# Kernel optimization log

Hardware: AMD Instinct MI355X
Metric: run time of the kernel (lower is better)

## Reference

```python
import jax, jax.numpy as jnp
import numpy as np

EMSIZE = 2048
NCLASS = 128
D1 = 2
D2 = 2
NSENT = 32768


def setup_inputs() -> dict:
    key = jax.random.key(0)
    k1, k2, k3 = jax.random.split(key, 3)
    x = jax.random.normal(k1, (NSENT, 1, EMSIZE), dtype=jnp.float32)
    # Scaled-normal params (original uses nn.init.normal_; scaling keeps tanh unsaturated)
    W1 = jax.random.normal(k2, (D1 + 1, EMSIZE, NCLASS), dtype=jnp.float32) / np.float32(np.sqrt(EMSIZE))
    b1 = jnp.zeros((1, NCLASS), dtype=jnp.float32)
    W2 = jax.random.normal(k3, (D2 + 1, NCLASS, NCLASS), dtype=jnp.float32) / np.float32(np.sqrt(NCLASS))
    b2 = jnp.zeros((1, NCLASS), dtype=jnp.float32)
    return {"structural_representations": x, "W1": W1, "b1": b1, "W2": W2, "b2": b2}


def _shift_down(y, k, n):
    # y[p] -> y[p-k], zeros for p < k (causal shift along sentence axis)
    return jnp.pad(y, ((k, 0), (0, 0)))[:n] if k > 0 else y


def reference(structural_representations, W1, b1, W2, b2):
    x = structural_representations  # [N, 1, E]
    n, _, e = x.shape
    d1 = W1.shape[0] - 1
    d2 = W2.shape[0] - 1
    c = W1.shape[-1]
    xs = x.reshape(n, e)  # [N, E]

    # Stage 1: S[p] = sum_{k=0..d1, k<=p} (x[p-k] @ W1[k] + b1)
    Y = jnp.einsum('ne,kec->knc', xs, W1)  # [d1+1, N, C]: one big GEMM per tap
    S = sum(_shift_down(Y[k], k, n) for k in range(d1 + 1))  # windowed causal sum
    pos = jnp.arange(n)
    cnt1 = (jnp.minimum(pos, d1) + 1).astype(xs.dtype)  # bias added once per valid tap
    H = jnp.tanh(S + cnt1[:, None] * b1[0])  # [N, C]

    # Stage 2 (i >= d2): Z[i] = sum_{j=0..d2} H[i-d2+j] @ W2[j] + (d2+1)*b2
    G = jnp.einsum('nc,kcd->knd', H, W2)  # [d2+1, N, C]
    Z = sum(_shift_down(G[j], d2 - j, n) for j in range(d2 + 1)) + (d2 + 1) * b2[0]

    # Fallback for i < d2: single term tanh(x[i]@W1[0]+b1) @ W2[0] + b2
    H0 = jnp.tanh(xs @ W1[0] + b1[0])
    Z0 = H0 @ W2[0] + b2[0]
    Z = jnp.where((pos >= d2)[:, None], Z, Z0)

    out = jax.nn.log_softmax(Z, axis=-1)
    return out.reshape(n, 1, c)
```

## Files before the change

### kernel.cpp

```cpp
#include <hip/hip_runtime.h>
#include <math.h>

typedef __attribute__((ext_vector_type(8))) short short8;
typedef __attribute__((ext_vector_type(4))) float f32x4;

#define MFMA16(a, b, c) __builtin_amdgcn_mfma_f32_16x16x32_bf16((a), (b), (c), 0, 0, 0)

__device__ inline void gl_lds16(const void* g, void* l) {
  __builtin_amdgcn_global_load_lds(
      (const __attribute__((address_space(1))) void*)g,
      (__attribute__((address_space(3))) void*)l, 16, 0, 0);
}

__device__ inline unsigned int pack2(float lo, float hi) {
  unsigned int ulo = __float_as_uint(lo), uhi = __float_as_uint(hi);
  return (uhi & 0xFFFF0000u) | (ulo >> 16);
}
__device__ inline unsigned short f2bf_r(float f) {
  return (unsigned short)((__float_as_uint(f) + 0x8000u) >> 16);
}
__device__ inline float bf2f(unsigned short h) {
  return __uint_as_float(((unsigned int)h) << 16);
}

__global__ __launch_bounds__(256) void k_repack_w1(const float* __restrict__ W1,
                                                   unsigned short* __restrict__ W1bt) {
  __shared__ float tile[64 * 128];
  const int b = blockIdx.x;
  const int k = b >> 5, et = b & 31;
  const int e0 = et * 64;
  const int tid = threadIdx.x;
  const float* src = W1 + (size_t)k * 262144 + (size_t)e0 * 128;
#pragma unroll
  for (int i = 0; i < 8; ++i) {
    int idx4 = tid + i * 256;
    ((f32x4*)tile)[idx4] = ((const f32x4*)src)[idx4];
  }
  __syncthreads();
#pragma unroll
  for (int i = 0; i < 4; ++i) {
    int item = tid + i * 256;
    int c = item >> 3, eo = (item & 7) * 8;
    union { unsigned short h[8]; uint4 v; } t;
#pragma unroll
    for (int u = 0; u < 8; ++u) t.h[u] = f2bf_r(tile[(eo + u) * 128 + c]);
    *(uint4*)(W1bt + (size_t)(k * 128 + c) * 2048 + e0 + eo) = t.v;
  }
}

__global__ __launch_bounds__(256) void k_repack_w2(const float* __restrict__ W2,
                                                   unsigned short* __restrict__ W2t) {
  int idx = blockIdx.x * 256 + threadIdx.x;
  int j = idx >> 14, r = idx & 16383, d = r >> 7, c = r & 127;
  W2t[idx] = f2bf_r(W2[(size_t)j * 16384 + (size_t)c * 128 + d]);
}

__global__ __launch_bounds__(256, 2) void k_gemm1(const float* __restrict__ X,
                                                  const unsigned short* __restrict__ Bt,
                                                  unsigned short* __restrict__ Ybf) {
  __shared__ float Alds[64 * 64];
  __shared__ unsigned short Blds[384 * 64];

  const int r0 = blockIdx.x * 64;
  const int tid = threadIdx.x, wave = tid >> 6, lane = tid & 63;
  const int mrow = lane & 15, quad = lane >> 4;

  const float* agp[4];
#pragma unroll
  for (int r = 0; r < 4; ++r) {
    int row = wave * 16 + r * 4 + (lane >> 4);
    int c = (lane & 15) ^ (row & 15);
    agp[r] = X + (size_t)(r0 + row) * 2048 + c * 4;
  }
  const unsigned short* bgp[12];
#pragma unroll
  for (int r = 0; r < 12; ++r) {
    int col = wave * 96 + r * 8 + (lane >> 3);
    int c = (lane & 7) ^ (col & 7);
    bgp[r] = Bt + (size_t)col * 2048 + c * 8;
  }

  f32x4 acc[4][6] = {};

  for (int k0 = 0; k0 < 2048; k0 += 64) {
#pragma unroll
    for (int r = 0; r < 4; ++r)
      gl_lds16(agp[r], (char*)Alds + (wave * 16 + r * 4) * 256);
#pragma unroll
    for (int r = 0; r < 12; ++r)
      gl_lds16(bgp[r], (char*)Blds + (wave * 96 + r * 8) * 128);
#pragma unroll
    for (int r = 0; r < 4; ++r) agp[r] += 64;
#pragma unroll
    for (int r = 0; r < 12; ++r) bgp[r] += 64;
    __syncthreads();

#pragma unroll
    for (int s = 0; s < 2; ++s) {
      short8 af[4];
#pragma unroll
      for (int rt = 0; rt < 4; ++rt) {
        int row = rt * 16 + mrow;
        int c0 = s * 8 + quad * 2;
        const float* base = Alds + row * 64;
        f32x4 x0 = *(const f32x4*)(base + ((c0 ^ mrow) * 4));
        f32x4 x1 = *(const f32x4*)(base + (((c0 + 1) ^ mrow) * 4));
        union { unsigned int u[4]; short8 v; } t;
        t.u[0] = pack2(x0[0], x0[1]); t.u[1] = pack2(x0[2], x0[3]);
        t.u[2] = pack2(x1[0], x1[1]); t.u[3] = pack2(x1[2], x1[3]);
        af[rt] = t.v;
      }
#pragma unroll
      for (int ct = 0; ct < 6; ++ct) {
        int col = wave * 96 + ct * 16 + mrow;
        int ch = (s * 4 + quad) ^ (mrow & 7);
        short8 bf = *(const short8*)(Blds + col * 64 + ch * 8);
#pragma unroll
        for (int rt = 0; rt < 4; ++rt)
          acc[rt][ct] = MFMA16(af[rt], bf, acc[rt][ct]);
      }
    }
    __syncthreads();
  }

#pragma unroll
  for (int rt = 0; rt < 4; ++rt)
#pragma unroll
    for (int ct = 0; ct < 6; ++ct)
#pragma unroll
      for (int rg = 0; rg < 4; ++rg) {
        int rrow = r0 + rt * 16 + quad * 4 + rg;
        int ccol = wave * 96 + ct * 16 + mrow;
        Ybf[(size_t)rrow * 384 + ccol] = f2bf_r(acc[rt][ct][rg]);
      }
}

#define HS 136
__global__ __launch_bounds__(256) void k_stage2(const unsigned short* __restrict__ Yb,
                                                const unsigned short* __restrict__ W2t,
                                                const float* __restrict__ b1,
                                                const float* __restrict__ b2,
                                                float* __restrict__ out) {
  __shared__ unsigned short Hlds[66 * HS];
  __shared__ float zbuf[2][128];
  const int bid = blockIdx.x, tid = threadIdx.x;
  const int r0 = bid * 64;

  for (int idx = tid; idx < 66 * 128; idx += 256) {
    int hl = idx >> 7, c = idx & 127;
    int p = r0 - 2 + hl;
    float h = 0.f;
    if (p >= 0) {
      float s = bf2f(Yb[(size_t)p * 384 + c]);
      float cnt = 1.f;
      if (p >= 1) { s += bf2f(Yb[(size_t)(p - 1) * 384 + 128 + c]); cnt += 1.f; }
      if (p >= 2) { s += bf2f(Yb[(size_t)(p - 2) * 384 + 256 + c]); cnt += 1.f; }
      h = tanhf(fmaf(cnt, b1[c], s));
    }
    Hlds[hl * HS + c] = f2bf_r(h);
  }
  __syncthreads();

  const int wave = tid >> 6, lane = tid & 63, mrow = lane & 15, quad = lane >> 4;
  f32x4 acc[8] = {};
#pragma unroll
  for (int j = 0; j < 3; ++j) {
#pragma unroll
    for (int kk = 0; kk < 4; ++kk) {
      short8 a0 = *(const short8*)&Hlds[(wave * 16 + mrow + j) * HS + kk * 32 + quad * 8];
      const unsigned short* wp = W2t + (size_t)(j * 128 + mrow) * 128 + kk * 32 + quad * 8;
#pragma unroll
      for (int ct = 0; ct < 8; ++ct)
        acc[ct] = MFMA16(a0, *(const short8*)(wp + ct * 16 * 128), acc[ct]);
    }
  }

#pragma unroll
  for (int rg = 0; rg < 4; ++rg) {
    float z[8]; float m = -1e30f;
#pragma unroll
    for (int ct = 0; ct < 8; ++ct) {
      z[ct] = acc[ct][rg] + 3.f * b2[ct * 16 + mrow];
      m = fmaxf(m, z[ct]);
    }
#pragma unroll
    for (int off = 1; off < 16; off <<= 1) m = fmaxf(m, __shfl_xor(m, off, 64));
    float s = 0.f;
#pragma unroll
    for (int ct = 0; ct < 8; ++ct) s += __expf(z[ct] - m);
#pragma unroll
    for (int off = 1; off < 16; off <<= 1) s += __shfl_xor(s, off, 64);
    float lse = m + __logf(s);
    int grow = r0 + wave * 16 + quad * 4 + rg;
    if (grow >= 2) {
      float* op = out + (size_t)grow * 128 + mrow;
#pragma unroll
      for (int ct = 0; ct < 8; ++ct) op[ct * 16] = z[ct] - lse;
    }
  }

  if (bid == 0) {
    __syncthreads();
    int row = tid >> 7, d = tid & 127;
    zbuf[row][d] = tanhf(bf2f(Yb[(size_t)row * 384 + d]) + b1[d]);
    __syncthreads();
    float zv = b2[d];
    for (int c = 0; c < 128; ++c)
      zv = fmaf(zbuf[row][c], bf2f(W2t[(size_t)d * 128 + c]), zv);
    __syncthreads();
    zbuf[row][d] = zv;
    __syncthreads();
    float m = -1e30f;
    for (int c = 0; c < 128; ++c) m = fmaxf(m, zbuf[row][c]);
    float s = 0.f;
    for (int c = 0; c < 128; ++c) s += __expf(zbuf[row][c] - m);
    out[(size_t)row * 128 + d] = zv - m - __logf(s);
  }
}

extern "C" void kernel_launch(void* const* d_in, const int* in_sizes, int n_in,
                              void* d_out, int out_size, void* d_ws, size_t ws_size,
                              hipStream_t stream) {
  const float* X  = (const float*)d_in[0];
  const float* W1 = (const float*)d_in[1];
  const float* b1 = (const float*)d_in[2];
  const float* W2 = (const float*)d_in[3];
  const float* b2 = (const float*)d_in[4];
  float* out = (float*)d_out;

  unsigned short* Ybf  = (unsigned short*)d_ws;
  unsigned short* W1bt = (unsigned short*)((char*)d_ws + 25165824);
  unsigned short* W2t  = (unsigned short*)((char*)d_ws + 25165824 + 1572864);

  k_repack_w1<<<96, 256, 0, stream>>>(W1, W1bt);
  k_repack_w2<<<192, 256, 0, stream>>>(W2, W2t);
  k_gemm1<<<512, 256, 0, stream>>>(X, W1bt, Ybf);
  k_stage2<<<512, 256, 0, stream>>>(Ybf, W2t, b1, b2, out);
}
```

Before: 460.5 us.

## Fuse stage-1 GEMM with stage-2 via recomputed halo rows and merge repack kernels

Merges the GEMM1 and stage-2 kernels into one: each block recomputes 4 extra halo rows of the first GEMM so the causal window and the second GEMM can read Y from LDS. This removes the bf16 Y round trip through global memory (about 25 MB written and read back) and one kernel launch. The two weight repack kernels are also merged into one launch. The cost is 25% more GEMM1 MFMA work per block, more LDS (66 KB), and higher register pressure from the 5x6 accumulators, which can lower occupancy.

```diff
diff --git a/kernel.cpp b/kernel.cpp
--- a/kernel.cpp
+++ b/kernel.cpp
@@ -23,54 +23,66 @@
   return __uint_as_float(((unsigned int)h) << 16);
 }
 
-__global__ __launch_bounds__(256) void k_repack_w1(const float* __restrict__ W1,
-                                                   unsigned short* __restrict__ W1bt) {
+__global__ __launch_bounds__(256) void k_repack(const float* __restrict__ W1,
+                                                const float* __restrict__ W2,
+                                                unsigned short* __restrict__ W1bt,
+                                                unsigned short* __restrict__ W2t) {
   __shared__ float tile[64 * 128];
-  const int b = blockIdx.x;
-  const int k = b >> 5, et = b & 31;
-  const int e0 = et * 64;
-  const int tid = threadIdx.x;
-  const float* src = W1 + (size_t)k * 262144 + (size_t)e0 * 128;
-#pragma unroll
-  for (int i = 0; i < 8; ++i) {
-    int idx4 = tid + i * 256;
-    ((f32x4*)tile)[idx4] = ((const f32x4*)src)[idx4];
-  }
-  __syncthreads();
-#pragma unroll
-  for (int i = 0; i < 4; ++i) {
-    int item = tid + i * 256;
-    int c = item >> 3, eo = (item & 7) * 8;
-    union { unsigned short h[8]; uint4 v; } t;
-#pragma unroll
-    for (int u = 0; u < 8; ++u) t.h[u] = f2bf_r(tile[(eo + u) * 128 + c]);
-    *(uint4*)(W1bt + (size_t)(k * 128 + c) * 2048 + e0 + eo) = t.v;
-  }
-}
-
-__global__ __launch_bounds__(256) void k_repack_w2(const float* __restrict__ W2,
-                                                   unsigned short* __restrict__ W2t) {
-  int idx = blockIdx.x * 256 + threadIdx.x;
-  int j = idx >> 14, r = idx & 16383, d = r >> 7, c = r & 127;
-  W2t[idx] = f2bf_r(W2[(size_t)j * 16384 + (size_t)c * 128 + d]);
-}
-
-__global__ __launch_bounds__(256, 2) void k_gemm1(const float* __restrict__ X,
+  const int b = blockIdx.x, tid = threadIdx.x;
+  if (b < 96) {
+    const int k = b >> 5, et = b & 31;
+    const int e0 = et * 64;
+    const float* src = W1 + (size_t)k * 262144 + (size_t)e0 * 128;
+#pragma unroll
+    for (int i = 0; i < 8; ++i) {
+      int idx4 = tid + i * 256;
+      ((f32x4*)tile)[idx4] = ((const f32x4*)src)[idx4];
+    }
+    __syncthreads();
+#pragma unroll
+    for (int i = 0; i < 4; ++i) {
+      int item = tid + i * 256;
+      int c = item >> 3, eo = (item & 7) * 8;
+      union { unsigned short h[8]; uint4 v; } t;
+#pragma unroll
+      for (int u = 0; u < 8; ++u) t.h[u] = f2bf_r(tile[(eo + u) * 128 + c]);
+      *(uint4*)(W1bt + (size_t)(k * 128 + c) * 2048 + e0 + eo) = t.v;
+    }
+  } else {
+    int idx = (b - 96) * 256 + tid;
+    int j = idx >> 14, r = idx & 16383, d = r >> 7, c = r & 127;
+    W2t[idx] = f2bf_r(W2[(size_t)j * 16384 + (size_t)c * 128 + d]);
+  }
+}
+
+__global__ __launch_bounds__(256, 2) void k_fused(const float* __restrict__ X,
                                                   const unsigned short* __restrict__ Bt,
-                                                  unsigned short* __restrict__ Ybf) {
-  __shared__ float Alds[64 * 64];
-  __shared__ unsigned short Blds[384 * 64];
+                                                  const unsigned short* __restrict__ W2t,
+                                                  const float* __restrict__ b1,
+                                                  const float* __restrict__ b2,
+                                                  float* __restrict__ out) {
+  __shared__ __align__(16) char smem[66560];
+  float* Alds = (float*)smem;
+  unsigned short* Blds = (unsigned short*)(smem + 17408);
+  unsigned short* Yt = (unsigned short*)smem;
+  float* zbuf = (float*)(smem + 62720);
 
   const int r0 = blockIdx.x * 64;
   const int tid = threadIdx.x, wave = tid >> 6, lane = tid & 63;
   const int mrow = lane & 15, quad = lane >> 4;
 
-  const float* agp[4];
+  const float* agp[5];
 #pragma unroll
   for (int r = 0; r < 4; ++r) {
-    int row = wave * 16 + r * 4 + (lane >> 4);
-    int c = (lane & 15) ^ (row & 15);
-    agp[r] = X + (size_t)(r0 + row) * 2048 + c * 4;
+    int i = wave * 16 + r * 4 + (lane >> 4);
+    int g = r0 - 4 + i; if (g < 0) g = 0;
+    int c = (lane & 15) ^ (i & 15);
+    agp[r] = X + (size_t)g * 2048 + c * 4;
+  }
+  {
+    int i = 64 + (lane >> 4);
+    int c = (lane & 15) ^ (i & 15);
+    agp[4] = X + (size_t)(r0 - 4 + i) * 2048 + c * 4;
   }
   const unsigned short* bgp[12];
 #pragma unroll
@@ -80,26 +92,27 @@
     bgp[r] = Bt + (size_t)col * 2048 + c * 8;
   }
 
-  f32x4 acc[4][6] = {};
+  f32x4 acc[5][6] = {};
 
   for (int k0 = 0; k0 < 2048; k0 += 64) {
 #pragma unroll
     for (int r = 0; r < 4; ++r)
       gl_lds16(agp[r], (char*)Alds + (wave * 16 + r * 4) * 256);
+    if (wave == 0) gl_lds16(agp[4], (char*)Alds + 64 * 256);
 #pragma unroll
     for (int r = 0; r < 12; ++r)
       gl_lds16(bgp[r], (char*)Blds + (wave * 96 + r * 8) * 128);
 #pragma unroll
-    for (int r = 0; r < 4; ++r) agp[r] += 64;
+    for (int r = 0; r < 5; ++r) agp[r] += 64;
 #pragma unroll
     for (int r = 0; r < 12; ++r) bgp[r] += 64;
     __syncthreads();
 
 #pragma unroll
     for (int s = 0; s < 2; ++s) {
-      short8 af[4];
-#pragma unroll
-      for (int rt = 0; rt < 4; ++rt) {
+      short8 af[5];
+#pragma unroll
+      for (int rt = 0; rt < 5; ++rt) {
         int row = rt * 16 + mrow;
         int c0 = s * 8 + quad * 2;
         const float* base = Alds + row * 64;
@@ -116,7 +129,7 @@
         int ch = (s * 4 + quad) ^ (mrow & 7);
         short8 bf = *(const short8*)(Blds + col * 64 + ch * 8);
 #pragma unroll
-        for (int rt = 0; rt < 4; ++rt)
+        for (int rt = 0; rt < 5; ++rt)
           acc[rt][ct] = MFMA16(af[rt], bf, acc[rt][ct]);
       }
     }
@@ -124,54 +137,43 @@
   }
 
 #pragma unroll
-  for (int rt = 0; rt < 4; ++rt)
+  for (int rt = 0; rt < 5; ++rt)
 #pragma unroll
     for (int ct = 0; ct < 6; ++ct)
 #pragma unroll
       for (int rg = 0; rg < 4; ++rg) {
-        int rrow = r0 + rt * 16 + quad * 4 + rg;
-        int ccol = wave * 96 + ct * 16 + mrow;
-        Ybf[(size_t)rrow * 384 + ccol] = f2bf_r(acc[rt][ct][rg]);
+        int l = rt * 16 + quad * 4 + rg;
+        int col = wave * 96 + ct * 16 + mrow;
+        Yt[l * 392 + col] = f2bf_r(acc[rt][ct][rg]);
       }
-}
-
-#define HS 136
-__global__ __launch_bounds__(256) void k_stage2(const unsigned short* __restrict__ Yb,
-                                                const unsigned short* __restrict__ W2t,
-                                                const float* __restrict__ b1,
-                                                const float* __restrict__ b2,
-                                                float* __restrict__ out) {
-  __shared__ unsigned short Hlds[66 * HS];
-  __shared__ float zbuf[2][128];
-  const int bid = blockIdx.x, tid = threadIdx.x;
-  const int r0 = bid * 64;
+  __syncthreads();
 
   for (int idx = tid; idx < 66 * 128; idx += 256) {
     int hl = idx >> 7, c = idx & 127;
     int p = r0 - 2 + hl;
+    int i = hl + 2;
     float h = 0.f;
     if (p >= 0) {
-      float s = bf2f(Yb[(size_t)p * 384 + c]);
+      float s = bf2f(Yt[i * 392 + c]);
       float cnt = 1.f;
-      if (p >= 1) { s += bf2f(Yb[(size_t)(p - 1) * 384 + 128 + c]); cnt += 1.f; }
-      if (p >= 2) { s += bf2f(Yb[(size_t)(p - 2) * 384 + 256 + c]); cnt += 1.f; }
+      if (p >= 1) { s += bf2f(Yt[(i - 1) * 392 + 128 + c]); cnt += 1.f; }
+      if (p >= 2) { s += bf2f(Yt[(i - 2) * 392 + 256 + c]); cnt += 1.f; }
       h = tanhf(fmaf(cnt, b1[c], s));
     }
-    Hlds[hl * HS + c] = f2bf_r(h);
+    Yt[(i - 2) * 392 + 256 + c] = f2bf_r(h);
   }
   __syncthreads();
 
-  const int wave = tid >> 6, lane = tid & 63, mrow = lane & 15, quad = lane >> 4;
-  f32x4 acc[8] = {};
+  f32x4 acc2[8] = {};
 #pragma unroll
   for (int j = 0; j < 3; ++j) {
 #pragma unroll
     for (int kk = 0; kk < 4; ++kk) {
-      short8 a0 = *(const short8*)&Hlds[(wave * 16 + mrow + j) * HS + kk * 32 + quad * 8];
+      short8 a0 = *(const short8*)&Yt[(wave * 16 + mrow + j) * 392 + 256 + kk * 32 + quad * 8];
       const unsigned short* wp = W2t + (size_t)(j * 128 + mrow) * 128 + kk * 32 + quad * 8;
 #pragma unroll
       for (int ct = 0; ct < 8; ++ct)
-        acc[ct] = MFMA16(a0, *(const short8*)(wp + ct * 16 * 128), acc[ct]);
+        acc2[ct] = MFMA16(a0, *(const short8*)(wp + ct * 16 * 128), acc2[ct]);
     }
   }
 
@@ -180,7 +182,7 @@
     float z[8]; float m = -1e30f;
 #pragma unroll
     for (int ct = 0; ct < 8; ++ct) {
-      z[ct] = acc[ct][rg] + 3.f * b2[ct * 16 + mrow];
+      z[ct] = acc2[ct][rg] + 3.f * b2[ct * 16 + mrow];
       m = fmaxf(m, z[ct]);
     }
 #pragma unroll
@@ -199,21 +201,21 @@
     }
   }
 
-  if (bid == 0) {
+  if (blockIdx.x == 0) {
     __syncthreads();
     int row = tid >> 7, d = tid & 127;
-    zbuf[row][d] = tanhf(bf2f(Yb[(size_t)row * 384 + d]) + b1[d]);
+    zbuf[row * 128 + d] = tanhf(bf2f(Yt[(row + 4) * 392 + d]) + b1[d]);
     __syncthreads();
     float zv = b2[d];
     for (int c = 0; c < 128; ++c)
-      zv = fmaf(zbuf[row][c], bf2f(W2t[(size_t)d * 128 + c]), zv);
-    __syncthreads();
-    zbuf[row][d] = zv;
+      zv = fmaf(zbuf[row * 128 + c], bf2f(W2t[(size_t)d * 128 + c]), zv);
+    __syncthreads();
+    zbuf[row * 128 + d] = zv;
     __syncthreads();
     float m = -1e30f;
-    for (int c = 0; c < 128; ++c) m = fmaxf(m, zbuf[row][c]);
+    for (int c = 0; c < 128; ++c) m = fmaxf(m, zbuf[row * 128 + c]);
     float s = 0.f;
-    for (int c = 0; c < 128; ++c) s += __expf(zbuf[row][c] - m);
+    for (int c = 0; c < 128; ++c) s += __expf(zbuf[row * 128 + c] - m);
     out[(size_t)row * 128 + d] = zv - m - __logf(s);
   }
 }
@@ -228,12 +230,9 @@
   const float* b2 = (const float*)d_in[4];
   float* out = (float*)d_out;
 
-  unsigned short* Ybf  = (unsigned short*)d_ws;
-  unsigned short* W1bt = (unsigned short*)((char*)d_ws + 25165824);
-  unsigned short* W2t  = (unsigned short*)((char*)d_ws + 25165824 + 1572864);
-
-  k_repack_w1<<<96, 256, 0, stream>>>(W1, W1bt);
-  k_repack_w2<<<192, 256, 0, stream>>>(W2, W2t);
-  k_gemm1<<<512, 256, 0, stream>>>(X, W1bt, Ybf);
-  k_stage2<<<512, 256, 0, stream>>>(Ybf, W2t, b1, b2, out);
-}
+  unsigned short* W1bt = (unsigned short*)d_ws;
+  unsigned short* W2t  = (unsigned short*)((char*)d_ws + 1572864);
+
+  k_repack<<<288, 256, 0, stream>>>(W1, W2, W1bt, W2t);
+  k_fused<<<512, 256, 0, stream>>>(X, W1bt, W2t, b1, b2, out);
+}
```

Measured after the change: 425.4 us. 7.6% less time.

## Double-buffer GEMM1 LDS tiles, convert X to bf16 on load, merge repack kernels

Applied to the files above, without the earlier changes.

The first-stage GEMM now uses 512-thread blocks covering 128 rows, arranged as a 2x4 wave grid. The A and B tiles are double-buffered in LDS so the next K-slice loads while the current one is multiplied. X is converted from fp32 to bf16 in registers before it is written to LDS, which halves A's LDS footprint and removes the repeated per-wave packing of A. The two weight-repack kernels are merged into one launch to cut launch overhead. The risk is that the synchronous register path for A is no longer an async global-to-LDS copy and may stall waves, and the larger LDS use (about 128KB per block) limits occupancy.

```diff
diff --git a/kernel.cpp b/kernel.cpp
--- a/kernel.cpp
+++ b/kernel.cpp
@@ -23,103 +23,115 @@
   return __uint_as_float(((unsigned int)h) << 16);
 }
 
-__global__ __launch_bounds__(256) void k_repack_w1(const float* __restrict__ W1,
-                                                   unsigned short* __restrict__ W1bt) {
+__global__ __launch_bounds__(256) void k_repack(const float* __restrict__ W1,
+                                                const float* __restrict__ W2,
+                                                unsigned short* __restrict__ W1bt,
+                                                unsigned short* __restrict__ W2t) {
   __shared__ float tile[64 * 128];
-  const int b = blockIdx.x;
-  const int k = b >> 5, et = b & 31;
-  const int e0 = et * 64;
-  const int tid = threadIdx.x;
-  const float* src = W1 + (size_t)k * 262144 + (size_t)e0 * 128;
-#pragma unroll
-  for (int i = 0; i < 8; ++i) {
-    int idx4 = tid + i * 256;
-    ((f32x4*)tile)[idx4] = ((const f32x4*)src)[idx4];
-  }
-  __syncthreads();
-#pragma unroll
-  for (int i = 0; i < 4; ++i) {
-    int item = tid + i * 256;
-    int c = item >> 3, eo = (item & 7) * 8;
-    union { unsigned short h[8]; uint4 v; } t;
-#pragma unroll
-    for (int u = 0; u < 8; ++u) t.h[u] = f2bf_r(tile[(eo + u) * 128 + c]);
-    *(uint4*)(W1bt + (size_t)(k * 128 + c) * 2048 + e0 + eo) = t.v;
-  }
-}
-
-__global__ __launch_bounds__(256) void k_repack_w2(const float* __restrict__ W2,
-                                                   unsigned short* __restrict__ W2t) {
-  int idx = blockIdx.x * 256 + threadIdx.x;
-  int j = idx >> 14, r = idx & 16383, d = r >> 7, c = r & 127;
-  W2t[idx] = f2bf_r(W2[(size_t)j * 16384 + (size_t)c * 128 + d]);
-}
-
-__global__ __launch_bounds__(256, 2) void k_gemm1(const float* __restrict__ X,
+  const int b = blockIdx.x, tid = threadIdx.x;
+  if (b < 96) {
+    const int k = b >> 5, et = b & 31;
+    const int e0 = et * 64;
+    const float* src = W1 + (size_t)k * 262144 + (size_t)e0 * 128;
+#pragma unroll
+    for (int i = 0; i < 8; ++i) {
+      int idx4 = tid + i * 256;
+      ((f32x4*)tile)[idx4] = ((const f32x4*)src)[idx4];
+    }
+    __syncthreads();
+#pragma unroll
+    for (int i = 0; i < 4; ++i) {
+      int item = tid + i * 256;
+      int c = item >> 3, eo = (item & 7) * 8;
+      union { unsigned short h[8]; uint4 v; } t;
+#pragma unroll
+      for (int u = 0; u < 8; ++u) t.h[u] = f2bf_r(tile[(eo + u) * 128 + c]);
+      *(uint4*)(W1bt + (size_t)(k * 128 + c) * 2048 + e0 + eo) = t.v;
+    }
+  } else {
+    int idx = (b - 96) * 256 + tid;
+    int j = idx >> 14, r = idx & 16383, d = r >> 7, c = r & 127;
+    W2t[idx] = f2bf_r(W2[(size_t)j * 16384 + (size_t)c * 128 + d]);
+  }
+}
+
+__global__ __launch_bounds__(512, 2) void k_gemm1(const float* __restrict__ X,
                                                   const unsigned short* __restrict__ Bt,
                                                   unsigned short* __restrict__ Ybf) {
-  __shared__ float Alds[64 * 64];
-  __shared__ unsigned short Blds[384 * 64];
-
-  const int r0 = blockIdx.x * 64;
+  __shared__ __align__(16) unsigned short Albuf[2][128 * 64];
+  __shared__ __align__(16) unsigned short Blbuf[2][384 * 64];
+
+  const int r0 = blockIdx.x * 128;
   const int tid = threadIdx.x, wave = tid >> 6, lane = tid & 63;
   const int mrow = lane & 15, quad = lane >> 4;
-
-  const float* agp[4];
-#pragma unroll
-  for (int r = 0; r < 4; ++r) {
-    int row = wave * 16 + r * 4 + (lane >> 4);
-    int c = (lane & 15) ^ (row & 15);
-    agp[r] = X + (size_t)(r0 + row) * 2048 + c * 4;
-  }
-  const unsigned short* bgp[12];
-#pragma unroll
-  for (int r = 0; r < 12; ++r) {
-    int col = wave * 96 + r * 8 + (lane >> 3);
+  const int rg = wave >> 2, cg = wave & 3;
+
+  const unsigned short* bsrc[6];
+#pragma unroll
+  for (int r = 0; r < 6; ++r) {
+    int col = wave * 48 + r * 8 + (lane >> 3);
     int c = (lane & 7) ^ (col & 7);
-    bgp[r] = Bt + (size_t)col * 2048 + c * 8;
-  }
+    bsrc[r] = Bt + (size_t)col * 2048 + c * 8;
+  }
+  const int arow = wave * 16 + (lane >> 2);
+  const float* asrc = X + (size_t)(r0 + arow) * 2048 + (lane & 3) * 16;
+  const int ac0 = (lane & 3) * 2;
+  const int aslot0 = ac0 ^ (arow & 7), aslot1 = (ac0 + 1) ^ (arow & 7);
 
   f32x4 acc[4][6] = {};
 
-  for (int k0 = 0; k0 < 2048; k0 += 64) {
-#pragma unroll
-    for (int r = 0; r < 4; ++r)
-      gl_lds16(agp[r], (char*)Alds + (wave * 16 + r * 4) * 256);
-#pragma unroll
-    for (int r = 0; r < 12; ++r)
-      gl_lds16(bgp[r], (char*)Blds + (wave * 96 + r * 8) * 128);
-#pragma unroll
-    for (int r = 0; r < 4; ++r) agp[r] += 64;
-#pragma unroll
-    for (int r = 0; r < 12; ++r) bgp[r] += 64;
-    __syncthreads();
-
+  auto stageB = [&](unsigned short* Bb, int k0) {
+#pragma unroll
+    for (int r = 0; r < 6; ++r)
+      gl_lds16(bsrc[r] + k0, (char*)Bb + (wave * 48 + r * 8) * 128);
+  };
+  auto stageA = [&](unsigned short* Ab, int k0) {
+    const float* s = asrc + k0;
+    f32x4 v0 = *(const f32x4*)(s);
+    f32x4 v1 = *(const f32x4*)(s + 4);
+    f32x4 v2 = *(const f32x4*)(s + 8);
+    f32x4 v3 = *(const f32x4*)(s + 12);
+    union { unsigned int u[4]; short8 h; } t0, t1;
+    t0.u[0] = pack2(v0[0], v0[1]); t0.u[1] = pack2(v0[2], v0[3]);
+    t0.u[2] = pack2(v1[0], v1[1]); t0.u[3] = pack2(v1[2], v1[3]);
+    t1.u[0] = pack2(v2[0], v2[1]); t1.u[1] = pack2(v2[2], v2[3]);
+    t1.u[2] = pack2(v3[0], v3[1]); t1.u[3] = pack2(v3[2], v3[3]);
+    *(short8*)(Ab + arow * 64 + aslot0 * 8) = t0.h;
+    *(short8*)(Ab + arow * 64 + aslot1 * 8) = t1.h;
+  };
+  auto compute = [&](const unsigned short* Ab, const unsigned short* Bb) {
 #pragma unroll
     for (int s = 0; s < 2; ++s) {
+      const int ch = (s * 4 + quad) ^ (mrow & 7);
       short8 af[4];
 #pragma unroll
-      for (int rt = 0; rt < 4; ++rt) {
-        int row = rt * 16 + mrow;
-        int c0 = s * 8 + quad * 2;
-        const float* base = Alds + row * 64;
-        f32x4 x0 = *(const f32x4*)(base + ((c0 ^ mrow) * 4));
-        f32x4 x1 = *(const f32x4*)(base + (((c0 + 1) ^ mrow) * 4));
-        union { unsigned int u[4]; short8 v; } t;
-        t.u[0] = pack2(x0[0], x0[1]); t.u[1] = pack2(x0[2], x0[3]);
-        t.u[2] = pack2(x1[0], x1[1]); t.u[3] = pack2(x1[2], x1[3]);
-        af[rt] = t.v;
-      }
+      for (int rt = 0; rt < 4; ++rt)
+        af[rt] = *(const short8*)(Ab + (rg * 64 + rt * 16 + mrow) * 64 + ch * 8);
 #pragma unroll
       for (int ct = 0; ct < 6; ++ct) {
-        int col = wave * 96 + ct * 16 + mrow;
-        int ch = (s * 4 + quad) ^ (mrow & 7);
-        short8 bf = *(const short8*)(Blds + col * 64 + ch * 8);
+        short8 bf = *(const short8*)(Bb + (cg * 96 + ct * 16 + mrow) * 64 + ch * 8);
 #pragma unroll
         for (int rt = 0; rt < 4; ++rt)
           acc[rt][ct] = MFMA16(af[rt], bf, acc[rt][ct]);
       }
     }
+  };
+
+  stageB(Blbuf[0], 0);
+  stageA(Albuf[0], 0);
+  __syncthreads();
+
+  for (int ii = 0; ii < 16; ++ii) {
+    const int k0 = ii * 128;
+    stageB(Blbuf[1], k0 + 64);
+    stageA(Albuf[1], k0 + 64);
+    compute(Albuf[0], Blbuf[0]);
+    __syncthreads();
+    if (k0 + 128 < 2048) {
+      stageB(Blbuf[0], k0 + 128);
+      stageA(Albuf[0], k0 + 128);
+    }
+    compute(Albuf[1], Blbuf[1]);
     __syncthreads();
   }
 
@@ -128,10 +140,10 @@
 #pragma unroll
     for (int ct = 0; ct < 6; ++ct)
 #pragma unroll
-      for (int rg = 0; rg < 4; ++rg) {
-        int rrow = r0 + rt * 16 + quad * 4 + rg;
-        int ccol = wave * 96 + ct * 16 + mrow;
-        Ybf[(size_t)rrow * 384 + ccol] = f2bf_r(acc[rt][ct][rg]);
+      for (int g = 0; g < 4; ++g) {
+        int row = r0 + rg * 64 + rt * 16 + quad * 4 + g;
+        int col = cg * 96 + ct * 16 + mrow;
+        Ybf[(size_t)row * 384 + col] = f2bf_r(acc[rt][ct][g]);
       }
 }
 
@@ -176,11 +188,11 @@
   }
 
 #pragma unroll
-  for (int rg = 0; rg < 4; ++rg) {
+  for (int rg2 = 0; rg2 < 4; ++rg2) {
     float z[8]; float m = -1e30f;
 #pragma unroll
     for (int ct = 0; ct < 8; ++ct) {
-      z[ct] = acc[ct][rg] + 3.f * b2[ct * 16 + mrow];
+      z[ct] = acc[ct][rg2] + 3.f * b2[ct * 16 + mrow];
       m = fmaxf(m, z[ct]);
     }
 #pragma unroll
@@ -191,7 +203,7 @@
 #pragma unroll
     for (int off = 1; off < 16; off <<= 1) s += __shfl_xor(s, off, 64);
     float lse = m + __logf(s);
-    int grow = r0 + wave * 16 + quad * 4 + rg;
+    int grow = r0 + wave * 16 + quad * 4 + rg2;
     if (grow >= 2) {
       float* op = out + (size_t)grow * 128 + mrow;
 #pragma unroll
@@ -232,8 +244,7 @@
   unsigned short* W1bt = (unsigned short*)((char*)d_ws + 25165824);
   unsigned short* W2t  = (unsigned short*)((char*)d_ws + 25165824 + 1572864);
 
-  k_repack_w1<<<96, 256, 0, stream>>>(W1, W1bt);
-  k_repack_w2<<<192, 256, 0, stream>>>(W2, W2t);
-  k_gemm1<<<512, 256, 0, stream>>>(X, W1bt, Ybf);
+  k_repack<<<288, 256, 0, stream>>>(W1, W2, W1bt, W2t);
+  k_gemm1<<<256, 512, 0, stream>>>(X, W1bt, Ybf);
   k_stage2<<<512, 256, 0, stream>>>(Ybf, W2t, b1, b2, out);
 }
```

After: 462.5 us. Within noise of the previous version (+0.4%).

## Double-buffer A tiles in LDS and read W1 directly from global in GEMM1

Applied to the files above, without the earlier changes.

The first GEMM now stages only the fp32 X tile through LDS, using two buffers of 128-wide K chunks so the next chunk loads while the current one is computed. B fragments come straight from global memory (and L2) instead of being staged in LDS, which removes B's LDS traffic and halves the number of barriers per K. The two weight repack kernels are merged into one launch. The trade-off is that direct global B loads sit on the MFMA critical path, and the larger LDS footprint may reduce occupancy.

```diff
diff --git a/kernel.cpp b/kernel.cpp
--- a/kernel.cpp
+++ b/kernel.cpp
@@ -23,115 +23,118 @@
   return __uint_as_float(((unsigned int)h) << 16);
 }
 
-__global__ __launch_bounds__(256) void k_repack_w1(const float* __restrict__ W1,
-                                                   unsigned short* __restrict__ W1bt) {
+__global__ __launch_bounds__(256) void k_repack(const float* __restrict__ W1,
+                                                const float* __restrict__ W2,
+                                                unsigned short* __restrict__ W1bt,
+                                                unsigned short* __restrict__ W2t) {
   __shared__ float tile[64 * 128];
-  const int b = blockIdx.x;
-  const int k = b >> 5, et = b & 31;
-  const int e0 = et * 64;
-  const int tid = threadIdx.x;
-  const float* src = W1 + (size_t)k * 262144 + (size_t)e0 * 128;
-#pragma unroll
-  for (int i = 0; i < 8; ++i) {
-    int idx4 = tid + i * 256;
-    ((f32x4*)tile)[idx4] = ((const f32x4*)src)[idx4];
-  }
-  __syncthreads();
-#pragma unroll
-  for (int i = 0; i < 4; ++i) {
-    int item = tid + i * 256;
-    int c = item >> 3, eo = (item & 7) * 8;
-    union { unsigned short h[8]; uint4 v; } t;
-#pragma unroll
-    for (int u = 0; u < 8; ++u) t.h[u] = f2bf_r(tile[(eo + u) * 128 + c]);
-    *(uint4*)(W1bt + (size_t)(k * 128 + c) * 2048 + e0 + eo) = t.v;
-  }
-}
-
-__global__ __launch_bounds__(256) void k_repack_w2(const float* __restrict__ W2,
-                                                   unsigned short* __restrict__ W2t) {
-  int idx = blockIdx.x * 256 + threadIdx.x;
-  int j = idx >> 14, r = idx & 16383, d = r >> 7, c = r & 127;
-  W2t[idx] = f2bf_r(W2[(size_t)j * 16384 + (size_t)c * 128 + d]);
+  const int b = blockIdx.x, tid = threadIdx.x;
+  if (b < 96) {
+    const int k = b >> 5, et = b & 31;
+    const int e0 = et * 64;
+    const float* src = W1 + (size_t)k * 262144 + (size_t)e0 * 128;
+#pragma unroll
+    for (int i = 0; i < 8; ++i) {
+      int idx4 = tid + i * 256;
+      ((f32x4*)tile)[idx4] = ((const f32x4*)src)[idx4];
+    }
+    __syncthreads();
+#pragma unroll
+    for (int i = 0; i < 4; ++i) {
+      int item = tid + i * 256;
+      int c = item >> 3, eo = (item & 7) * 8;
+      union { unsigned short h[8]; uint4 v; } t;
+#pragma unroll
+      for (int u = 0; u < 8; ++u) t.h[u] = f2bf_r(tile[(eo + u) * 128 + c]);
+      *(uint4*)(W1bt + (size_t)(k * 128 + c) * 2048 + e0 + eo) = t.v;
+    }
+  } else {
+    int idx = (b - 96) * 256 + tid;
+    int j = idx >> 14, r = idx & 16383, d = r >> 7, c = r & 127;
+    W2t[idx] = f2bf_r(W2[(size_t)j * 16384 + (size_t)c * 128 + d]);
+  }
 }
 
 __global__ __launch_bounds__(256, 2) void k_gemm1(const float* __restrict__ X,
                                                   const unsigned short* __restrict__ Bt,
                                                   unsigned short* __restrict__ Ybf) {
-  __shared__ float Alds[64 * 64];
-  __shared__ unsigned short Blds[384 * 64];
+  __shared__ __align__(16) float Albuf[2][64 * 128];
 
   const int r0 = blockIdx.x * 64;
   const int tid = threadIdx.x, wave = tid >> 6, lane = tid & 63;
   const int mrow = lane & 15, quad = lane >> 4;
 
-  const float* agp[4];
-#pragma unroll
-  for (int r = 0; r < 4; ++r) {
-    int row = wave * 16 + r * 4 + (lane >> 4);
-    int c = (lane & 15) ^ (row & 15);
+  const float* agp[8];
+#pragma unroll
+  for (int r = 0; r < 8; ++r) {
+    int call = wave * 8 + r;
+    int row = call * 2 + (lane >> 5);
+    int c = (lane & 31) ^ (row & 15);
     agp[r] = X + (size_t)(r0 + row) * 2048 + c * 4;
   }
-  const unsigned short* bgp[12];
-#pragma unroll
-  for (int r = 0; r < 12; ++r) {
-    int col = wave * 96 + r * 8 + (lane >> 3);
-    int c = (lane & 7) ^ (col & 7);
-    bgp[r] = Bt + (size_t)col * 2048 + c * 8;
+
+  const unsigned short* bptr[6];
+#pragma unroll
+  for (int ct = 0; ct < 6; ++ct) {
+    int col = wave * 96 + ct * 16 + mrow;
+    bptr[ct] = Bt + (size_t)col * 2048 + quad * 8;
   }
 
   f32x4 acc[4][6] = {};
 
-  for (int k0 = 0; k0 < 2048; k0 += 64) {
-#pragma unroll
-    for (int r = 0; r < 4; ++r)
-      gl_lds16(agp[r], (char*)Alds + (wave * 16 + r * 4) * 256);
-#pragma unroll
-    for (int r = 0; r < 12; ++r)
-      gl_lds16(bgp[r], (char*)Blds + (wave * 96 + r * 8) * 128);
-#pragma unroll
-    for (int r = 0; r < 4; ++r) agp[r] += 64;
-#pragma unroll
-    for (int r = 0; r < 12; ++r) bgp[r] += 64;
-    __syncthreads();
-
-#pragma unroll
-    for (int s = 0; s < 2; ++s) {
+  auto stageA = [&](float* Ab, int k0) {
+#pragma unroll
+    for (int r = 0; r < 8; ++r)
+      gl_lds16(agp[r] + k0, (char*)Ab + (wave * 8 + r) * 1024);
+  };
+  auto compute = [&](const float* Ab, int k0) {
+#pragma unroll
+    for (int kk = 0; kk < 4; ++kk) {
+      short8 bf[6];
+#pragma unroll
+      for (int ct = 0; ct < 6; ++ct)
+        bf[ct] = *(const short8*)(bptr[ct] + k0 + kk * 32);
       short8 af[4];
 #pragma unroll
       for (int rt = 0; rt < 4; ++rt) {
-        int row = rt * 16 + mrow;
-        int c0 = s * 8 + quad * 2;
-        const float* base = Alds + row * 64;
+        int c0 = kk * 8 + quad * 2;
+        const float* base = Ab + (rt * 16 + mrow) * 128;
         f32x4 x0 = *(const f32x4*)(base + ((c0 ^ mrow) * 4));
         f32x4 x1 = *(const f32x4*)(base + (((c0 + 1) ^ mrow) * 4));
-        union { unsigned int u[4]; short8 v; } t;
+        union { unsigned int u[4]; short8 h; } t;
         t.u[0] = pack2(x0[0], x0[1]); t.u[1] = pack2(x0[2], x0[3]);
         t.u[2] = pack2(x1[0], x1[1]); t.u[3] = pack2(x1[2], x1[3]);
-        af[rt] = t.v;
+        af[rt] = t.h;
       }
 #pragma unroll
-      for (int ct = 0; ct < 6; ++ct) {
+      for (int ct = 0; ct < 6; ++ct)
+#pragma unroll
+        for (int rt = 0; rt < 4; ++rt)
+          acc[rt][ct] = MFMA16(af[rt], bf[ct], acc[rt][ct]);
+    }
+  };
+
+  stageA(Albuf[0], 0);
+  __syncthreads();
+  for (int ii = 0; ii < 8; ++ii) {
+    const int k0 = ii * 256;
+    stageA(Albuf[1], k0 + 128);
+    compute(Albuf[0], k0);
+    __syncthreads();
+    if (k0 + 256 < 2048) stageA(Albuf[0], k0 + 256);
+    compute(Albuf[1], k0 + 128);
+    __syncthreads();
+  }
+
+#pragma unroll
+  for (int rt = 0; rt < 4; ++rt)
+#pragma unroll
+    for (int ct = 0; ct < 6; ++ct)
+#pragma unroll
+      for (int g = 0; g < 4; ++g) {
+        int row = r0 + rt * 16 + quad * 4 + g;
         int col = wave * 96 + ct * 16 + mrow;
-        int ch = (s * 4 + quad) ^ (mrow & 7);
-        short8 bf = *(const short8*)(Blds + col * 64 + ch * 8);
-#pragma unroll
-        for (int rt = 0; rt < 4; ++rt)
-          acc[rt][ct] = MFMA16(af[rt], bf, acc[rt][ct]);
-      }
-    }
-    __syncthreads();
-  }
-
-#pragma unroll
-  for (int rt = 0; rt < 4; ++rt)
-#pragma unroll
-    for (int ct = 0; ct < 6; ++ct)
-#pragma unroll
-      for (int rg = 0; rg < 4; ++rg) {
-        int rrow = r0 + rt * 16 + quad * 4 + rg;
-        int ccol = wave * 96 + ct * 16 + mrow;
-        Ybf[(size_t)rrow * 384 + ccol] = f2bf_r(acc[rt][ct][rg]);
+        Ybf[(size_t)row * 384 + col] = f2bf_r(acc[rt][ct][g]);
       }
 }
 
@@ -176,11 +179,11 @@
   }
 
 #pragma unroll
-  for (int rg = 0; rg < 4; ++rg) {
+  for (int rg2 = 0; rg2 < 4; ++rg2) {
     float z[8]; float m = -1e30f;
 #pragma unroll
     for (int ct = 0; ct < 8; ++ct) {
-      z[ct] = acc[ct][rg] + 3.f * b2[ct * 16 + mrow];
+      z[ct] = acc[ct][rg2] + 3.f * b2[ct * 16 + mrow];
       m = fmaxf(m, z[ct]);
     }
 #pragma unroll
@@ -191,7 +194,7 @@
 #pragma unroll
     for (int off = 1; off < 16; off <<= 1) s += __shfl_xor(s, off, 64);
     float lse = m + __logf(s);
-    int grow = r0 + wave * 16 + quad * 4 + rg;
+    int grow = r0 + wave * 16 + quad * 4 + rg2;
     if (grow >= 2) {
       float* op = out + (size_t)grow * 128 + mrow;
 #pragma unroll
@@ -232,8 +235,7 @@
   unsigned short* W1bt = (unsigned short*)((char*)d_ws + 25165824);
   unsigned short* W2t  = (unsigned short*)((char*)d_ws + 25165824 + 1572864);
 
-  k_repack_w1<<<96, 256, 0, stream>>>(W1, W1bt);
-  k_repack_w2<<<192, 256, 0, stream>>>(W2, W2t);
+  k_repack<<<288, 256, 0, stream>>>(W1, W2, W1bt, W2t);
   k_gemm1<<<512, 256, 0, stream>>>(X, W1bt, Ybf);
   k_stage2<<<512, 256, 0, stream>>>(Ybf, W2t, b1, b2, out);
 }
```

Result: slower. 493.0 us (+7.0%).
